# Optimization experiments

Hardware: AMD Instinct MI355X
Metric: run time of the kernel (lower is better)

Reference implementation:

```python
import jax, jax.numpy as jnp
import numpy as np

N = 131072        # number of points
S = 16384         # number of groups (segments)
D_IN = 256        # fea_dims[0]
NUM_RF = 1024     # random-feature width
D_OUT = 128       # fea_dims[1] (embedding dim)
_INV_SQRT2 = 1.0 / np.sqrt(2.0).astype(np.float32)
_INV_SQRT2PI = 1.0 / np.sqrt(2.0 * np.pi).astype(np.float32)


def setup_inputs() -> dict:
    key = jax.random.key(0)
    k1, k2, k3, k4, k5, k6 = jax.random.split(key, 6)
    X = jax.random.normal(k1, (N, D_IN), dtype=jnp.float32)
    # balanced group assignment (guarantees no empty segment -> no inf/nan)
    X_idx = jax.random.permutation(k2, jnp.arange(N, dtype=jnp.int64) % S)
    W1_mu = jax.random.normal(k3, (NUM_RF, D_IN), dtype=jnp.float32) * 0.05
    W1_var = jax.random.uniform(k4, (NUM_RF, D_IN), dtype=jnp.float32) * 0.01 + 1e-4
    W2_mu = jax.random.normal(k5, (D_OUT, NUM_RF), dtype=jnp.float32) * 0.05
    W2_var = jax.random.uniform(k6, (D_OUT, NUM_RF), dtype=jnp.float32) * 0.01 + 1e-4
    return {"X": X, "X_idx": X_idx, "W1_mu": W1_mu, "W1_var": W1_var,
            "W2_mu": W2_mu, "W2_var": W2_var}


def _vb_linear(m, v, W_mu, W_var):
    # Variational Bayes linear layer: propagate mean/variance through
    # independent Gaussian weights W ~ N(W_mu, W_var).
    mo = m @ W_mu.T                                   # [N, out]
    if v is None:
        vo = (m * m) @ W_var.T
    else:
        vo = v @ (W_mu * W_mu).T + (m * m + v) @ W_var.T
    return mo, vo


def _relu_moments(mu, var):
    # Exact first/second moments of ReLU of a Gaussian N(mu, var).
    s = jnp.sqrt(var + 1e-8)
    z = mu / s
    Phi = 0.5 * (1.0 + jax.scipy.special.erf(z * _INV_SQRT2))
    phi = jnp.exp(-0.5 * z * z) * _INV_SQRT2PI
    m_out = mu * Phi + s * phi
    e_y2 = (mu * mu + var) * Phi + mu * s * phi
    v_out = jnp.maximum(e_y2 - m_out * m_out, 1e-6)
    return m_out, v_out


def reference(X, X_idx, W1_mu, W1_var, W2_mu, W2_var):
    # DGP-RF block: D_IN -> NUM_RF (ReLU moments) -> D_OUT
    m, v = _vb_linear(X, None, W1_mu, W1_var)         # [N, NUM_RF]
    m, v = _relu_moments(m, v)
    out_means, out_vars = _vb_linear(m, v, W2_mu, W2_var)  # [N, D_OUT]
    # Precision-weighted aggregation over X_idx groups (Gaussian product)
    prec = 1.0 / out_vars                              # [N, D_OUT]
    embedd_vars = 1.0 / jax.ops.segment_sum(prec, X_idx, num_segments=S)
    embedd_means = jax.ops.segment_sum(prec * out_means, X_idx, num_segments=S)
    embedd_means = embedd_means * embedd_vars          # [S, D_OUT]
    return embedd_means, embedd_vars
```

## Files before the change

kernel.cpp:

```cpp
#include <hip/hip_runtime.h>


#define NPTS   131072
#define SGRP   16384
#define DIN    256
#define NRF    1024
#define DOUT   128
#define MT     64
#define NWG    (NPTS / MT)

#define XLD    264
#define XQLD   264
#define TMLD   72
#define TVLD   72

typedef unsigned short ushort_t;
typedef unsigned char  uchar_t;
typedef __attribute__((ext_vector_type(8))) short bf16x8;
typedef __attribute__((ext_vector_type(4))) float f32x4;
typedef __attribute__((ext_vector_type(4))) float f32x4v;

__device__ __forceinline__ unsigned short f2bf(float f) {
  unsigned u = __float_as_uint(f);
  u += 0x7fffu + ((u >> 16) & 1u);
  return (unsigned short)(u >> 16);
}

template <bool HI>
__device__ __forceinline__ unsigned cvt2_fp8(float a, float b, unsigned old) {
#if __has_builtin(__builtin_amdgcn_cvt_pk_fp8_f32)
  return __builtin_amdgcn_cvt_pk_fp8_f32(a, b, old, HI);
#else
  auto enc = [](float x) -> unsigned {
    if (!(x > 0.00097656f)) return 0u;
    if (x >= 448.f) return 0x7Eu;
    union { float f; unsigned u; } v; v.f = x;
    int e = (int)(v.u >> 23) - 127;
    if (e < -6) { int n = (int)(x * 512.f + 0.5f); return (unsigned)n; }
    v.u += 0x0007FFFFu + ((v.u >> 20) & 1u);
    e = (int)(v.u >> 23) - 127;
    if (e > 8) return 0x7Eu;
    return (unsigned)(((e + 7) << 3) | ((v.u >> 20) & 7u));
  };
  unsigned p = (enc(a) | (enc(b) << 8));
  return HI ? ((old & 0x0000ffffu) | (p << 16)) : ((old & 0xffff0000u) | p);
#endif
}

__device__ __forceinline__ float fast_rcp(float x) {
#if __has_builtin(__builtin_amdgcn_rcpf)
  return __builtin_amdgcn_rcpf(x);
#else
  return 1.0f / x;
#endif
}
__device__ __forceinline__ float fast_rsq(float x) {
#if __has_builtin(__builtin_amdgcn_rsqf)
  return __builtin_amdgcn_rsqf(x);
#else
  return rsqrtf(x);
#endif
}

__global__ void detect_idx_kernel(const unsigned* __restrict__ raw,
                                  int* __restrict__ flag) {
  __shared__ int any_nz;
  if (threadIdx.x == 0) any_nz = 0;
  __syncthreads();
  if (raw[2 * threadIdx.x + 1] != 0u) atomicOr(&any_nz, 1);
  __syncthreads();
  if (threadIdx.x == 0) *flag = (any_nz == 0) ? 1 : 0;
}

__global__ void moments_table_kernel(float4* __restrict__ tab) {
  int i = threadIdx.x;
  float z0 = (float)i * 0.0625f - 8.0f;
  float h[2], w[2];
#pragma unroll
  for (int j = 0; j < 2; ++j) {
    float z = z0 + 0.0625f * j;
    float Phi = 0.5f * (1.0f + erff(z * 0.70710678118654752f));
    float phi = 0.3989422804014327f * expf(-0.5f * z * z);
    float hh = z * Phi + phi;
    float gg = (z * z + 1.0f) * Phi + z * phi;
    h[j] = hh;
    w[j] = gg - hh * hh;
  }
  tab[i] = make_float4(h[0], h[1] - h[0], w[0], w[1] - w[0]);
}

__global__ __launch_bounds__(256) void convert_kernel(
    const float* __restrict__ W1mu, const float* __restrict__ W1var,
    const float* __restrict__ W2mu, const float* __restrict__ W2var,
    ushort_t* __restrict__ w1mu_bf, uchar_t* __restrict__ w1var8,
    ushort_t* __restrict__ w2mu_bf, uchar_t* __restrict__ w2b8,
    uchar_t* __restrict__ w2var8) {
  int i4 = (blockIdx.x * 256 + threadIdx.x) * 4;
  {
    f32x4v m = *(const f32x4v*)(W1mu + i4);
    ushort4 b; b.x = f2bf(m[0]); b.y = f2bf(m[1]); b.z = f2bf(m[2]); b.w = f2bf(m[3]);
    *(ushort4*)(w1mu_bf + i4) = b;
    f32x4v v = *(const f32x4v*)(W1var + i4);
    unsigned p = cvt2_fp8<false>(v[0] * 256.f, v[1] * 256.f, 0u);
    p = cvt2_fp8<true>(v[2] * 256.f, v[3] * 256.f, p);
    *(unsigned*)(w1var8 + i4) = p;
  }
  if (i4 < NRF * DOUT) {
    f32x4v m = *(const f32x4v*)(W2mu + i4);
    f32x4v v = *(const f32x4v*)(W2var + i4);
    ushort4 b; b.x = f2bf(m[0]); b.y = f2bf(m[1]); b.z = f2bf(m[2]); b.w = f2bf(m[3]);
    *(ushort4*)(w2mu_bf + i4) = b;
    unsigned pb = cvt2_fp8<false>(fmaf(m[0], m[0], v[0]) * 256.f,
                                  fmaf(m[1], m[1], v[1]) * 256.f, 0u);
    pb = cvt2_fp8<true>(fmaf(m[2], m[2], v[2]) * 256.f,
                        fmaf(m[3], m[3], v[3]) * 256.f, pb);
    *(unsigned*)(w2b8 + i4) = pb;
    unsigned pv = cvt2_fp8<false>(v[0] * 256.f, v[1] * 256.f, 0u);
    pv = cvt2_fp8<true>(v[2] * 256.f, v[3] * 256.f, pv);
    *(unsigned*)(w2var8 + i4) = pv;
  }
}

__global__ __launch_bounds__(256, 2) void fused_kernel(
    const float* __restrict__ X,
    const unsigned* __restrict__ Xidx_raw,
    const ushort_t* __restrict__ W1mu, const uchar_t* __restrict__ W1var8,
    const ushort_t* __restrict__ W2mu, const uchar_t* __restrict__ W2b8,
    const uchar_t* __restrict__ W2var8,
    const float4* __restrict__ htab_g,
    const int* __restrict__ flag64,
    float* __restrict__ acc_means, float* __restrict__ acc_vars) {
  __shared__ ushort_t Xb[MT * XLD];
  __shared__ uchar_t  Xq8[MT * XQLD];
  __shared__ ushort_t Tm[MT * TMLD];
  __shared__ uchar_t  Tv8[MT * TVLD];
  __shared__ uchar_t  T38[MT * TVLD];
  __shared__ float4   htab[256];
  __shared__ int sidx[MT];

  const int tid = threadIdx.x;
  const int p0  = blockIdx.x * MT;
  const int is64 = *flag64;

  if (tid < MT) {
    int p = p0 + tid;
    sidx[tid] = (int)(is64 ? Xidx_raw[2 * (size_t)p] : Xidx_raw[p]);
  }
  htab[tid] = htab_g[tid];
#pragma unroll
  for (int i = 0; i < 16; ++i) {
    int idx4 = i * 256 + tid;
    int row  = idx4 >> 6;
    int c4   = idx4 & 63;
    f32x4v xv = *(const f32x4v*)(X + (size_t)(p0 + row) * DIN + c4 * 4);
    ushort4 b;
    b.x = f2bf(xv[0]); b.y = f2bf(xv[1]); b.z = f2bf(xv[2]); b.w = f2bf(xv[3]);
    *(ushort4*)(Xb + row * XLD + c4 * 4) = b;
    unsigned q = cvt2_fp8<false>(xv[0] * xv[0], xv[1] * xv[1], 0u);
    q = cvt2_fp8<true>(xv[2] * xv[2], xv[3] * xv[3], q);
    *(unsigned*)(Xq8 + row * XQLD + c4 * 4) = q;
  }
  __syncthreads();

  const int lane = tid & 63;
  const int wave = tid >> 6;
  const int l16  = lane & 15;
  const int quad = lane >> 4;
  const int qoff = quad * 8;

  const int nrow0 = (wave * 2 + 0) * 16 + l16;
  const int nrow1 = (wave * 2 + 1) * 16 + l16;

  f32x4 acc_mo[4][2], acc_vo[4][2];
#pragma unroll
  for (int mt = 0; mt < 4; ++mt)
#pragma unroll
    for (int j = 0; j < 2; ++j) {
      acc_mo[mt][j] = (f32x4){0.f, 0.f, 0.f, 0.f};
      acc_vo[mt][j] = (f32x4){0.f, 0.f, 0.f, 0.f};
    }

#pragma unroll 1
  for (int c = 0; c < 16; ++c) {
    const ushort_t* w1m = W1mu  + (size_t)(c * 64 + wave * 16 + l16) * DIN + qoff;
    const uchar_t*  w1v = W1var8 + (size_t)(c * 64 + wave * 16 + l16) * DIN + qoff;
    bf16x8 bmu[8]; long long bvr[8];
#pragma unroll
    for (int k = 0; k < 8; ++k) {
      bmu[k] = *(const bf16x8*)(w1m + k * 32);
      bvr[k] = *(const long long*)(w1v + k * 32);
    }
    f32x4 am[4], av[4];
#pragma unroll
    for (int mt = 0; mt < 4; ++mt) {
      am[mt] = (f32x4){0.f, 0.f, 0.f, 0.f};
      av[mt] = (f32x4){0.f, 0.f, 0.f, 0.f};
    }
#pragma unroll
    for (int k = 0; k < 8; ++k) {
#pragma unroll
      for (int mt = 0; mt < 4; ++mt) {
        bf16x8 ax = *(const bf16x8*)(Xb + (mt * 16 + l16) * XLD + k * 32 + qoff);
        long long aq = *(const long long*)(Xq8 + (mt * 16 + l16) * XQLD + k * 32 + qoff);
        am[mt] = __builtin_amdgcn_mfma_f32_16x16x32_bf16(ax, bmu[k], am[mt], 0, 0, 0);
        av[mt] = __builtin_amdgcn_mfma_f32_16x16x32_fp8_fp8(aq, bvr[k], av[mt], 0, 0, 0);
      }
    }

    const ushort_t* w2m0 = W2mu + (size_t)nrow0 * NRF + c * 64 + qoff;
    const ushort_t* w2m1 = W2mu + (size_t)nrow1 * NRF + c * 64 + qoff;
    const uchar_t* w2b0 = W2b8 + (size_t)nrow0 * NRF + c * 64 + qoff;
    const uchar_t* w2b1 = W2b8 + (size_t)nrow1 * NRF + c * 64 + qoff;
    const uchar_t* w2v0 = W2var8 + (size_t)nrow0 * NRF + c * 64 + qoff;
    const uchar_t* w2v1 = W2var8 + (size_t)nrow1 * NRF + c * 64 + qoff;
    bf16x8 b2m[2][2]; long long b2b[2][2], b2v[2][2];
#pragma unroll
    for (int k2 = 0; k2 < 2; ++k2) {
      b2m[0][k2] = *(const bf16x8*)(w2m0 + k2 * 32);
      b2m[1][k2] = *(const bf16x8*)(w2m1 + k2 * 32);
      b2b[0][k2] = *(const long long*)(w2b0 + k2 * 32);
      b2b[1][k2] = *(const long long*)(w2b1 + k2 * 32);
      b2v[0][k2] = *(const long long*)(w2v0 + k2 * 32);
      b2v[1][k2] = *(const long long*)(w2v1 + k2 * 32);
    }

    __syncthreads();

    const int col = wave * 16 + l16;
#pragma unroll
    for (int mt = 0; mt < 4; ++mt) {
#pragma unroll
      for (int r = 0; r < 4; ++r) {
        float mu  = am[mt][r];
        float vpe = fmaf(av[mt][r], 0.00390625f, 1e-8f);
        float rsq = fast_rsq(vpe);
        float z   = mu * rsq;
        float s   = vpe * rsq;
        float zc  = fminf(fmaxf(z, -8.0f), 7.96875f);
        float u   = fmaf(zc, 16.0f, 128.0f);
        float fu  = floorf(u);
        float f   = u - fu;
        float4 hv = htab[(int)fu];
        float h   = fmaf(f, hv.y, hv.x);
        float w   = fmaf(f, hv.w, hv.z);
        float mo  = (z > 7.9f) ? mu : s * h;
        float vo  = fmaxf(vpe * w, 1e-6f);
        int row = mt * 16 + quad * 4 + r;
        Tm[row * TMLD + col] = f2bf(mo);
        Tv8[row * TVLD + col] = (uchar_t)(cvt2_fp8<false>(vo, vo, 0u) & 0xffu);
        T38[row * TVLD + col] = (uchar_t)(cvt2_fp8<false>(mo * mo, mo * mo, 0u) & 0xffu);
      }
    }
    __syncthreads();

#pragma unroll
    for (int k2 = 0; k2 < 2; ++k2) {
#pragma unroll
      for (int mt = 0; mt < 4; ++mt) {
        int ar = mt * 16 + l16;
        bf16x8 fam = *(const bf16x8*)(Tm + ar * TMLD + k2 * 32 + qoff);
        long long fav = *(const long long*)(Tv8 + ar * TVLD + k2 * 32 + qoff);
        long long f3  = *(const long long*)(T38 + ar * TVLD + k2 * 32 + qoff);
        acc_mo[mt][0] = __builtin_amdgcn_mfma_f32_16x16x32_bf16(fam, b2m[0][k2], acc_mo[mt][0], 0, 0, 0);
        acc_mo[mt][1] = __builtin_amdgcn_mfma_f32_16x16x32_bf16(fam, b2m[1][k2], acc_mo[mt][1], 0, 0, 0);
        acc_vo[mt][0] = __builtin_amdgcn_mfma_f32_16x16x32_fp8_fp8(fav, b2b[0][k2], acc_vo[mt][0], 0, 0, 0);
        acc_vo[mt][1] = __builtin_amdgcn_mfma_f32_16x16x32_fp8_fp8(fav, b2b[1][k2], acc_vo[mt][1], 0, 0, 0);
        acc_vo[mt][0] = __builtin_amdgcn_mfma_f32_16x16x32_fp8_fp8(f3, b2v[0][k2], acc_vo[mt][0], 0, 0, 0);
        acc_vo[mt][1] = __builtin_amdgcn_mfma_f32_16x16x32_fp8_fp8(f3, b2v[1][k2], acc_vo[mt][1], 0, 0, 0);
      }
    }
  }

#pragma unroll
  for (int mt = 0; mt < 4; ++mt)
#pragma unroll
    for (int j = 0; j < 2; ++j) {
      int dim = (wave * 2 + j) * 16 + l16;
#pragma unroll
      for (int r = 0; r < 4; ++r) {
        int prow = mt * 16 + quad * 4 + r;
        float mo = acc_mo[mt][j][r];
        float vo = fmaf(acc_vo[mt][j][r], 0.00390625f, 1e-6f);
        float prec = fast_rcp(vo);
        size_t o = (size_t)sidx[prow] * DOUT + dim;
        unsafeAtomicAdd(acc_means + o, prec * mo);
        unsafeAtomicAdd(acc_vars + o, prec);
      }
    }
}

__global__ __launch_bounds__(256) void finalize_kernel(float* __restrict__ means,
                                                       float* __restrict__ vars) {
  int i = blockIdx.x * 256 + threadIdx.x;
  float p  = vars[i];
  float pm = means[i];
  float var = 1.0f / p;
  means[i] = pm * var;
  vars[i]  = var;
}

extern "C" void kernel_launch(void* const* d_in, const int* in_sizes, int n_in,
                              void* d_out, int out_size, void* d_ws, size_t ws_size,
                              hipStream_t stream) {
  const float*    X     = (const float*)d_in[0];
  const unsigned* Xidx  = (const unsigned*)d_in[1];
  const float*    W1mu  = (const float*)d_in[2];
  const float*    W1var = (const float*)d_in[3];
  const float*    W2mu  = (const float*)d_in[4];
  const float*    W2var = (const float*)d_in[5];
  float* out = (float*)d_out;

  ushort_t* w1mu_bf = (ushort_t*)d_ws;
  uchar_t*  w1var8  = (uchar_t*)(w1mu_bf + NRF * DIN);
  ushort_t* w2mu_bf = (ushort_t*)(w1var8 + NRF * DIN);
  uchar_t*  w2b8    = (uchar_t*)(w2mu_bf + NRF * DOUT);
  uchar_t*  w2var8  = w2b8 + NRF * DOUT;
  float4*   htab    = (float4*)(w2var8 + NRF * DOUT);
  int* flag = (int*)(htab + 256);

  (void)hipMemsetAsync(d_out, 0, (size_t)out_size * sizeof(float), stream);
  detect_idx_kernel<<<1, 256, 0, stream>>>(Xidx, flag);
  moments_table_kernel<<<1, 256, 0, stream>>>(htab);
  convert_kernel<<<(NRF * DIN) / 4 / 256, 256, 0, stream>>>(
      W1mu, W1var, W2mu, W2var, w1mu_bf, w1var8, w2mu_bf, w2b8, w2var8);
  fused_kernel<<<NWG, 256, 0, stream>>>(
      X, Xidx, w1mu_bf, w1var8, w2mu_bf, w2b8, w2var8, htab, flag,
      out, out + (size_t)SGRP * DOUT);
  finalize_kernel<<<(SGRP * DOUT) / 256, 256, 0, stream>>>(
      out, out + (size_t)SGRP * DOUT);
}
```

Baseline: 668.6 us.

## Keep X tile in registers and split first GEMM by rows per wave

```diff
diff --git a/kernel.cpp b/kernel.cpp
--- a/kernel.cpp
+++ b/kernel.cpp
@@ -9,8 +9,6 @@
 #define MT     64
 #define NWG    (NPTS / MT)
 
-#define XLD    264
-#define XQLD   264
 #define TMLD   72
 #define TVLD   72
 
@@ -130,8 +128,6 @@
     const float4* __restrict__ htab_g,
     const int* __restrict__ flag64,
     float* __restrict__ acc_means, float* __restrict__ acc_vars) {
-  __shared__ ushort_t Xb[MT * XLD];
-  __shared__ uchar_t  Xq8[MT * XQLD];
   __shared__ ushort_t Tm[MT * TMLD];
   __shared__ uchar_t  Tv8[MT * TVLD];
   __shared__ uchar_t  T38[MT * TVLD];
@@ -147,20 +143,6 @@
     sidx[tid] = (int)(is64 ? Xidx_raw[2 * (size_t)p] : Xidx_raw[p]);
   }
   htab[tid] = htab_g[tid];
-#pragma unroll
-  for (int i = 0; i < 16; ++i) {
-    int idx4 = i * 256 + tid;
-    int row  = idx4 >> 6;
-    int c4   = idx4 & 63;
-    f32x4v xv = *(const f32x4v*)(X + (size_t)(p0 + row) * DIN + c4 * 4);
-    ushort4 b;
-    b.x = f2bf(xv[0]); b.y = f2bf(xv[1]); b.z = f2bf(xv[2]); b.w = f2bf(xv[3]);
-    *(ushort4*)(Xb + row * XLD + c4 * 4) = b;
-    unsigned q = cvt2_fp8<false>(xv[0] * xv[0], xv[1] * xv[1], 0u);
-    q = cvt2_fp8<true>(xv[2] * xv[2], xv[3] * xv[3], q);
-    *(unsigned*)(Xq8 + row * XQLD + c4 * 4) = q;
-  }
-  __syncthreads();
 
   const int lane = tid & 63;
   const int wave = tid >> 6;
@@ -168,6 +150,28 @@
   const int quad = lane >> 4;
   const int qoff = quad * 8;
 
+  bf16x8 axr[8]; long long aqr[8];
+  {
+    const float* xrow = X + (size_t)(p0 + wave * 16 + l16) * DIN;
+#pragma unroll
+    for (int k = 0; k < 8; ++k) {
+      f32x4v xa = *(const f32x4v*)(xrow + k * 32 + qoff);
+      f32x4v xb = *(const f32x4v*)(xrow + k * 32 + qoff + 4);
+      bf16x8 a;
+      a[0] = (short)f2bf(xa[0]); a[1] = (short)f2bf(xa[1]);
+      a[2] = (short)f2bf(xa[2]); a[3] = (short)f2bf(xa[3]);
+      a[4] = (short)f2bf(xb[0]); a[5] = (short)f2bf(xb[1]);
+      a[6] = (short)f2bf(xb[2]); a[7] = (short)f2bf(xb[3]);
+      axr[k] = a;
+      unsigned lo = cvt2_fp8<false>(xa[0] * xa[0], xa[1] * xa[1], 0u);
+      lo = cvt2_fp8<true>(xa[2] * xa[2], xa[3] * xa[3], lo);
+      unsigned hi = cvt2_fp8<false>(xb[0] * xb[0], xb[1] * xb[1], 0u);
+      hi = cvt2_fp8<true>(xb[2] * xb[2], xb[3] * xb[3], hi);
+      aqr[k] = (long long)(((unsigned long long)hi << 32) | (unsigned long long)lo);
+    }
+  }
+  __syncthreads();
+
   const int nrow0 = (wave * 2 + 0) * 16 + l16;
   const int nrow1 = (wave * 2 + 1) * 16 + l16;
 
@@ -182,28 +186,22 @@
 
 #pragma unroll 1
   for (int c = 0; c < 16; ++c) {
-    const ushort_t* w1m = W1mu  + (size_t)(c * 64 + wave * 16 + l16) * DIN + qoff;
-    const uchar_t*  w1v = W1var8 + (size_t)(c * 64 + wave * 16 + l16) * DIN + qoff;
-    bf16x8 bmu[8]; long long bvr[8];
+    const ushort_t* w1mB = W1mu   + (size_t)(c * 64 + l16) * DIN + qoff;
+    const uchar_t*  w1vB = W1var8 + (size_t)(c * 64 + l16) * DIN + qoff;
+    f32x4 am[4], av[4];
+#pragma unroll
+    for (int j = 0; j < 4; ++j) {
+      am[j] = (f32x4){0.f, 0.f, 0.f, 0.f};
+      av[j] = (f32x4){0.f, 0.f, 0.f, 0.f};
+    }
 #pragma unroll
     for (int k = 0; k < 8; ++k) {
-      bmu[k] = *(const bf16x8*)(w1m + k * 32);
-      bvr[k] = *(const long long*)(w1v + k * 32);
-    }
-    f32x4 am[4], av[4];
-#pragma unroll
-    for (int mt = 0; mt < 4; ++mt) {
-      am[mt] = (f32x4){0.f, 0.f, 0.f, 0.f};
-      av[mt] = (f32x4){0.f, 0.f, 0.f, 0.f};
-    }
-#pragma unroll
-    for (int k = 0; k < 8; ++k) {
-#pragma unroll
-      for (int mt = 0; mt < 4; ++mt) {
-        bf16x8 ax = *(const bf16x8*)(Xb + (mt * 16 + l16) * XLD + k * 32 + qoff);
-        long long aq = *(const long long*)(Xq8 + (mt * 16 + l16) * XQLD + k * 32 + qoff);
-        am[mt] = __builtin_amdgcn_mfma_f32_16x16x32_bf16(ax, bmu[k], am[mt], 0, 0, 0);
-        av[mt] = __builtin_amdgcn_mfma_f32_16x16x32_fp8_fp8(aq, bvr[k], av[mt], 0, 0, 0);
+#pragma unroll
+      for (int j = 0; j < 4; ++j) {
+        bf16x8 bmu = *(const bf16x8*)(w1mB + (size_t)(j * 16) * DIN + k * 32);
+        long long bvr = *(const long long*)(w1vB + (size_t)(j * 16) * DIN + k * 32);
+        am[j] = __builtin_amdgcn_mfma_f32_16x16x32_bf16(axr[k], bmu, am[j], 0, 0, 0);
+        av[j] = __builtin_amdgcn_mfma_f32_16x16x32_fp8_fp8(aqr[k], bvr, av[j], 0, 0, 0);
       }
     }
 
@@ -226,13 +224,12 @@
 
     __syncthreads();
 
-    const int col = wave * 16 + l16;
-#pragma unroll
-    for (int mt = 0; mt < 4; ++mt) {
+#pragma unroll
+    for (int j = 0; j < 4; ++j) {
 #pragma unroll
       for (int r = 0; r < 4; ++r) {
-        float mu  = am[mt][r];
-        float vpe = fmaf(av[mt][r], 0.00390625f, 1e-8f);
+        float mu  = am[j][r];
+        float vpe = fmaf(av[j][r], 0.00390625f, 1e-8f);
         float rsq = fast_rsq(vpe);
         float z   = mu * rsq;
         float s   = vpe * rsq;
@@ -245,7 +242,8 @@
         float w   = fmaf(f, hv.w, hv.z);
         float mo  = (z > 7.9f) ? mu : s * h;
         float vo  = fmaxf(vpe * w, 1e-6f);
-        int row = mt * 16 + quad * 4 + r;
+        int row = wave * 16 + quad * 4 + r;
+        int col = j * 16 + l16;
         Tm[row * TMLD + col] = f2bf(mo);
         Tv8[row * TVLD + col] = (uchar_t)(cvt2_fp8<false>(vo, vo, 0u) & 0xffu);
         T38[row * TVLD + col] = (uchar_t)(cvt2_fp8<false>(mo * mo, mo * mo, 0u) & 0xffu);
```

Result: slower. 1.296 ms (+93.8%).
